# Kernel tuning notes

Hardware: AMD Instinct MI355X
Metric: run time of the kernel (lower is better)

## Reference

```python
import jax, jax.numpy as jnp
import numpy as np

HIDDEN = 512
KEY_DIM = HIDDEN // 8  # 64
B, N, M = 8, 2048, 2048


def setup_inputs() -> dict:
    key = jax.random.key(0)
    kx, ky, kwq, kbq, kwk, kbk = jax.random.split(key, 6)
    s = 1.0 / np.sqrt(HIDDEN)
    return {
        "x": jax.random.normal(kx, (B, N, HIDDEN), dtype=jnp.float32),
        "y": jax.random.normal(ky, (B, M, HIDDEN), dtype=jnp.float32),
        "Wq": jax.random.uniform(kwq, (KEY_DIM, HIDDEN), minval=-s, maxval=s, dtype=jnp.float32),
        "bq": jax.random.uniform(kbq, (KEY_DIM,), minval=-s, maxval=s, dtype=jnp.float32),
        "Wk": jax.random.uniform(kwk, (KEY_DIM, HIDDEN), minval=-s, maxval=s, dtype=jnp.float32),
        "bk": jax.random.uniform(kbk, (KEY_DIM,), minval=-s, maxval=s, dtype=jnp.float32),
    }


def reference(x, y, Wq, bq, Wk, bk):
    # linear projections (torch Linear: x @ W^T + b)
    q = jnp.einsum("bnh,kh->bnk", x, Wq) + bq  # [B,N,K]
    k = jnp.einsum("bmh,kh->bmk", y, Wk) + bk  # [B,M,K]
    # pairwise squared distance [B,N,M]
    dist = (
        -2.0 * jnp.einsum("bnk,bmk->bnm", q, k)
        + jnp.sum(q * q, axis=-1)[:, :, None]
        + jnp.sum(k * k, axis=-1)[:, None, :]
    )
    # max over M of exp(-dist), keepdim -> [B,N,1]
    atweight = jnp.max(jnp.exp(-dist), axis=-1, keepdims=True)
    # outer product per batch -> [B,N,N]
    attention = jnp.einsum("bni,bmi->bnm", atweight, atweight)
    return attention
```

## Files before the change

kernel.cpp:

```cpp
#include <hip/hip_runtime.h>

#define B_    8
#define N_    2048
#define H_    512
#define K_    64
#define NROWS 16384
#define RTOT  32768

typedef __attribute__((ext_vector_type(8))) __bf16 bf16x8;
typedef __attribute__((ext_vector_type(4))) float  floatx4;

#define MFMA(a, b, c) __builtin_amdgcn_mfma_f32_16x16x32_bf16((a), (b), (c), 0, 0, 0)

__global__ __launch_bounds__(256) void wcvt_kernel(
    const float* __restrict__ Wq, const float* __restrict__ Wk,
    __bf16* __restrict__ Whilo)
{
    const int i = blockIdx.x * 256 + threadIdx.x;
    const bool isQ = i < 32768;
    const int off = isQ ? i : i - 32768;
    const float f = isQ ? Wq[off] : Wk[off];
    const __bf16 h = (__bf16)f;
    const __bf16 l = (__bf16)(f - (float)h);
    const int base = isQ ? 0 : 65536;
    Whilo[base + off] = h;
    Whilo[base + 32768 + off] = l;
}

__global__ __launch_bounds__(128) void proj_kernel(
    const float* __restrict__ x, const float* __restrict__ y,
    const __bf16* __restrict__ Whilo,
    const float* __restrict__ bq, const float* __restrict__ bk,
    __bf16* __restrict__ qh, __bf16* __restrict__ ql,
    float* __restrict__ sq)
{
    const int tid  = threadIdx.x;
    const int wv   = tid >> 6;
    const int lane = tid & 63;
    const int quad = lane >> 4;
    const int l16  = lane & 15;
    const int rowbase = blockIdx.x * 64 + wv * 32;
    const bool isQ = rowbase < NROWS;
    const float* __restrict__ X   = isQ ? x : y;
    const int xrow0 = isQ ? rowbase : rowbase - NROWS;
    const __bf16* __restrict__ Whi = Whilo + (isQ ? 0 : 2 * 32768);
    const __bf16* __restrict__ Wlo = Whi + 32768;
    const float* __restrict__ bias = isQ ? bq : bk;

    floatx4 acc[2][4];
    #pragma unroll
    for (int rt = 0; rt < 2; ++rt)
        #pragma unroll
        for (int ot = 0; ot < 4; ++ot)
            acc[rt][ot] = floatx4{0.f, 0.f, 0.f, 0.f};

    for (int it = 0; it < 16; ++it) {
        const int k0 = it * 32 + quad * 8;
        bf16x8 ahi[2], alo[2];
        #pragma unroll
        for (int rt = 0; rt < 2; ++rt) {
            const float4 f0 = *reinterpret_cast<const float4*>(
                &X[(size_t)(xrow0 + rt * 16 + l16) * H_ + k0]);
            const float4 f1 = *reinterpret_cast<const float4*>(
                &X[(size_t)(xrow0 + rt * 16 + l16) * H_ + k0 + 4]);
            const float fv[8] = {f0.x, f0.y, f0.z, f0.w, f1.x, f1.y, f1.z, f1.w};
            #pragma unroll
            for (int j = 0; j < 8; ++j) {
                const __bf16 h = (__bf16)fv[j];
                ahi[rt][j] = h;
                alo[rt][j] = (__bf16)(fv[j] - (float)h);
            }
        }
        bf16x8 bhi[4], blo[4];
        #pragma unroll
        for (int ot = 0; ot < 4; ++ot) {
            const int wrow = ot * 16 + l16;
            bhi[ot] = *reinterpret_cast<const bf16x8*>(&Whi[(size_t)wrow * H_ + k0]);
            blo[ot] = *reinterpret_cast<const bf16x8*>(&Wlo[(size_t)wrow * H_ + k0]);
        }
        #pragma unroll
        for (int rt = 0; rt < 2; ++rt)
            #pragma unroll
            for (int ot = 0; ot < 4; ++ot) {
                acc[rt][ot] = MFMA(ahi[rt], bhi[ot], acc[rt][ot]);
                acc[rt][ot] = MFMA(ahi[rt], blo[ot], acc[rt][ot]);
                acc[rt][ot] = MFMA(alo[rt], bhi[ot], acc[rt][ot]);
            }
    }

    float bv[4];
    #pragma unroll
    for (int ot = 0; ot < 4; ++ot) bv[ot] = bias[ot * 16 + l16];

    #pragma unroll
    for (int rt = 0; rt < 2; ++rt) {
        float ss[4] = {0.f, 0.f, 0.f, 0.f};
        #pragma unroll
        for (int ot = 0; ot < 4; ++ot)
            #pragma unroll
            for (int r = 0; r < 4; ++r) {
                const float qv = acc[rt][ot][r] + bv[ot];
                acc[rt][ot][r] = qv;
                ss[r] = fmaf(qv, qv, ss[r]);
            }
        #pragma unroll
        for (int off = 1; off < 16; off <<= 1)
            #pragma unroll
            for (int r = 0; r < 4; ++r)
                ss[r] += __shfl_xor(ss[r], off);
        const int row0 = rowbase + rt * 16 + quad * 4;
        if (l16 == 0) {
            #pragma unroll
            for (int r = 0; r < 4; ++r) sq[row0 + r] = ss[r];
        }
        #pragma unroll
        for (int ot = 0; ot < 4; ++ot)
            #pragma unroll
            for (int r = 0; r < 4; ++r) {
                const size_t idx = (size_t)(row0 + r) * K_ + ot * 16 + l16;
                const float qv = acc[rt][ot][r];
                const __bf16 h = (__bf16)qv;
                qh[idx] = h;
                ql[idx] = (__bf16)(qv - (float)h);
            }
    }
}

__global__ __launch_bounds__(128) void dist_kernel(
    const __bf16* __restrict__ qh, const __bf16* __restrict__ ql,
    const float* __restrict__ sq, float* __restrict__ wout)
{
    const int tid  = threadIdx.x;
    const int wv   = tid >> 6;
    const int lane = tid & 63;
    const int quad = lane >> 4;
    const int l16  = lane & 15;
    const int blk  = blockIdx.x;
    const int b    = blk >> 6;
    const int nrow = (blk & 63) * 32 + wv * 16;
    const size_t qrow = (size_t)(b * N_ + nrow + l16);

    const bf16x8 ahi0 = *reinterpret_cast<const bf16x8*>(&qh[qrow * K_ + quad * 8]);
    const bf16x8 ahi1 = *reinterpret_cast<const bf16x8*>(&qh[qrow * K_ + 32 + quad * 8]);
    const bf16x8 alo0 = *reinterpret_cast<const bf16x8*>(&ql[qrow * K_ + quad * 8]);
    const bf16x8 alo1 = *reinterpret_cast<const bf16x8*>(&ql[qrow * K_ + 32 + quad * 8]);

    const __bf16* __restrict__ kh = qh + (size_t)NROWS * K_;
    const __bf16* __restrict__ kl = ql + (size_t)NROWS * K_;
    const float*  __restrict__ kk = sq + NROWS;

    floatx4 runmin = floatx4{1e30f, 1e30f, 1e30f, 1e30f};

    #pragma unroll 2
    for (int ms = 0; ms < 128; ++ms) {
        const size_t krow = (size_t)(b * N_ + ms * 16 + l16);
        const bf16x8 bh0 = *reinterpret_cast<const bf16x8*>(&kh[krow * K_ + quad * 8]);
        const bf16x8 bh1 = *reinterpret_cast<const bf16x8*>(&kh[krow * K_ + 32 + quad * 8]);
        const bf16x8 bl0 = *reinterpret_cast<const bf16x8*>(&kl[krow * K_ + quad * 8]);
        const bf16x8 bl1 = *reinterpret_cast<const bf16x8*>(&kl[krow * K_ + 32 + quad * 8]);
        const float kkv = kk[b * N_ + ms * 16 + l16];

        floatx4 acc = floatx4{0.f, 0.f, 0.f, 0.f};
        acc = MFMA(ahi0, bh0, acc);
        acc = MFMA(ahi1, bh1, acc);
        acc = MFMA(ahi0, bl0, acc);
        acc = MFMA(ahi1, bl1, acc);
        acc = MFMA(alo0, bh0, acc);
        acc = MFMA(alo1, bh1, acc);

        #pragma unroll
        for (int r = 0; r < 4; ++r) {
            const float d = fmaf(-2.f, acc[r], kkv);
            runmin[r] = fminf(runmin[r], d);
        }
    }

    #pragma unroll
    for (int off = 1; off < 16; off <<= 1)
        #pragma unroll
        for (int r = 0; r < 4; ++r)
            runmin[r] = fminf(runmin[r], __shfl_xor(runmin[r], off));

    if (l16 == 0) {
        #pragma unroll
        for (int r = 0; r < 4; ++r) {
            const int row = nrow + quad * 4 + r;
            const float d = runmin[r] + sq[b * N_ + row];
            wout[b * N_ + row] = expf(-d);
        }
    }
}

__global__ __launch_bounds__(256) void outer_kernel(
    const float* __restrict__ w, float4* __restrict__ out)
{
    const int f = blockIdx.x * 256 + threadIdx.x;
    const int m4 = f & 511;
    const int n  = (f >> 9) & 2047;
    const int b  = f >> 20;
    const float wn = w[(b << 11) + n];
    const float4 wm = reinterpret_cast<const float4*>(w)[(b << 9) + m4];
    float4 o;
    o.x = wn * wm.x; o.y = wn * wm.y; o.z = wn * wm.z; o.w = wn * wm.w;
    out[f] = o;
}

extern "C" void kernel_launch(void* const* d_in, const int* in_sizes, int n_in,
                              void* d_out, int out_size, void* d_ws, size_t ws_size,
                              hipStream_t stream)
{
    const float* x  = (const float*)d_in[0];
    const float* y  = (const float*)d_in[1];
    const float* Wq = (const float*)d_in[2];
    const float* bq = (const float*)d_in[3];
    const float* Wk = (const float*)d_in[4];
    const float* bk = (const float*)d_in[5];
    float* out = (float*)d_out;

    char* ws = (char*)d_ws;
    __bf16* qh    = (__bf16*)ws;
    __bf16* ql    = (__bf16*)(ws + 4194304);
    float*  sq    = (float*)(ws + 8388608);
    __bf16* Whilo = (__bf16*)(ws + 8519680);
    float*  w     = (float*)(ws + 8781824);

    wcvt_kernel<<<256, 256, 0, stream>>>(Wq, Wk, Whilo);
    proj_kernel<<<512, 128, 0, stream>>>(x, y, Whilo, bq, bk, qh, ql, sq);
    dist_kernel<<<512, 128, 0, stream>>>(qh, ql, sq, w);
    outer_kernel<<<32768, 256, 0, stream>>>(w, (float4*)out);
}
```

Before: 262.6 us.

## Fuse all stages into one cooperative kernel with split-M atomic min

Replaces the four separate launches with a single cooperative kernel that uses grid-wide syncs between weight conversion, projection, distance-min and outer-product phases. The distance phase splits the M range across two waves per row tile and combines them with an integer atomicMin on float bits, which doubles the number of waves. Projection uses 16-row tiles per wave for more parallelism. The outer product caches the batch weight vector in shared memory. The atomicMin on float bits assumes non-negative distances, and the grid syncs add some overhead.

```diff
diff --git a/kernel.cpp b/kernel.cpp
--- a/kernel.cpp
+++ b/kernel.cpp
@@ -1,4 +1,7 @@
 #include <hip/hip_runtime.h>
+#include <hip/hip_cooperative_groups.h>
+
+namespace cg = cooperative_groups;
 
 #define B_    8
 #define N_    2048
@@ -6,109 +9,103 @@
 #define K_    64
 #define NROWS 16384
 #define RTOT  32768
+#define NBLK  512
+#define NTHR  256
 
 typedef __attribute__((ext_vector_type(8))) __bf16 bf16x8;
 typedef __attribute__((ext_vector_type(4))) float  floatx4;
 
 #define MFMA(a, b, c) __builtin_amdgcn_mfma_f32_16x16x32_bf16((a), (b), (c), 0, 0, 0)
 
-__global__ __launch_bounds__(256) void wcvt_kernel(
-    const float* __restrict__ Wq, const float* __restrict__ Wk,
-    __bf16* __restrict__ Whilo)
+__global__ __launch_bounds__(NTHR, 2) void fused_kernel(
+    const float* __restrict__ x, const float* __restrict__ y,
+    const float* __restrict__ Wq, const float* __restrict__ bq,
+    const float* __restrict__ Wk, const float* __restrict__ bk,
+    float* __restrict__ out,
+    __bf16* __restrict__ qh, __bf16* __restrict__ ql,
+    float* __restrict__ sq, __bf16* __restrict__ Whilo,
+    int* __restrict__ minT)
 {
-    const int i = blockIdx.x * 256 + threadIdx.x;
-    const bool isQ = i < 32768;
-    const int off = isQ ? i : i - 32768;
-    const float f = isQ ? Wq[off] : Wk[off];
-    const __bf16 h = (__bf16)f;
-    const __bf16 l = (__bf16)(f - (float)h);
-    const int base = isQ ? 0 : 65536;
-    Whilo[base + off] = h;
-    Whilo[base + 32768 + off] = l;
-}
-
-__global__ __launch_bounds__(128) void proj_kernel(
-    const float* __restrict__ x, const float* __restrict__ y,
-    const __bf16* __restrict__ Whilo,
-    const float* __restrict__ bq, const float* __restrict__ bk,
-    __bf16* __restrict__ qh, __bf16* __restrict__ ql,
-    float* __restrict__ sq)
-{
+    cg::grid_group grid = cg::this_grid();
     const int tid  = threadIdx.x;
-    const int wv   = tid >> 6;
+    const int blk  = blockIdx.x;
+    const int gid  = blk * NTHR + tid;
     const int lane = tid & 63;
     const int quad = lane >> 4;
     const int l16  = lane & 15;
-    const int rowbase = blockIdx.x * 64 + wv * 32;
-    const bool isQ = rowbase < NROWS;
-    const float* __restrict__ X   = isQ ? x : y;
-    const int xrow0 = isQ ? rowbase : rowbase - NROWS;
-    const __bf16* __restrict__ Whi = Whilo + (isQ ? 0 : 2 * 32768);
-    const __bf16* __restrict__ Wlo = Whi + 32768;
-    const float* __restrict__ bias = isQ ? bq : bk;
-
-    floatx4 acc[2][4];
-    #pragma unroll
-    for (int rt = 0; rt < 2; ++rt)
-        #pragma unroll
-        for (int ot = 0; ot < 4; ++ot)
-            acc[rt][ot] = floatx4{0.f, 0.f, 0.f, 0.f};
-
-    for (int it = 0; it < 16; ++it) {
-        const int k0 = it * 32 + quad * 8;
-        bf16x8 ahi[2], alo[2];
-        #pragma unroll
-        for (int rt = 0; rt < 2; ++rt) {
+
+    if (gid < 2 * 32768) {
+        const bool isQ = gid < 32768;
+        const int off  = isQ ? gid : gid - 32768;
+        const float f  = isQ ? Wq[off] : Wk[off];
+        const __bf16 h = (__bf16)f;
+        const __bf16 l = (__bf16)(f - (float)h);
+        const int base = isQ ? 0 : 65536;
+        Whilo[base + off]         = h;
+        Whilo[base + 32768 + off] = l;
+    }
+    if (gid < NROWS) minT[gid] = 0x7f800000;
+    grid.sync();
+
+    {
+        const int wid = gid >> 6;
+        const int rowbase = wid * 16;
+        const bool isQ = rowbase < NROWS;
+        const float* __restrict__ X = isQ ? x : y;
+        const int xrow0 = isQ ? rowbase : rowbase - NROWS;
+        const __bf16* __restrict__ Whi = Whilo + (isQ ? 0 : 65536);
+        const __bf16* __restrict__ Wlo = Whi + 32768;
+        const float* __restrict__ bias = isQ ? bq : bk;
+
+        floatx4 acc[4];
+        #pragma unroll
+        for (int ot = 0; ot < 4; ++ot) acc[ot] = floatx4{0.f, 0.f, 0.f, 0.f};
+
+        for (int it = 0; it < 16; ++it) {
+            const int k0 = it * 32 + quad * 8;
             const float4 f0 = *reinterpret_cast<const float4*>(
-                &X[(size_t)(xrow0 + rt * 16 + l16) * H_ + k0]);
+                &X[(size_t)(xrow0 + l16) * H_ + k0]);
             const float4 f1 = *reinterpret_cast<const float4*>(
-                &X[(size_t)(xrow0 + rt * 16 + l16) * H_ + k0 + 4]);
+                &X[(size_t)(xrow0 + l16) * H_ + k0 + 4]);
             const float fv[8] = {f0.x, f0.y, f0.z, f0.w, f1.x, f1.y, f1.z, f1.w};
+            bf16x8 ahi, alo;
             #pragma unroll
             for (int j = 0; j < 8; ++j) {
                 const __bf16 h = (__bf16)fv[j];
-                ahi[rt][j] = h;
-                alo[rt][j] = (__bf16)(fv[j] - (float)h);
-            }
-        }
-        bf16x8 bhi[4], blo[4];
+                ahi[j] = h;
+                alo[j] = (__bf16)(fv[j] - (float)h);
+            }
+            #pragma unroll
+            for (int ot = 0; ot < 4; ++ot) {
+                const int wrow = ot * 16 + l16;
+                const bf16x8 bhi = *reinterpret_cast<const bf16x8*>(
+                    &Whi[(size_t)wrow * H_ + k0]);
+                const bf16x8 blo = *reinterpret_cast<const bf16x8*>(
+                    &Wlo[(size_t)wrow * H_ + k0]);
+                acc[ot] = MFMA(ahi, bhi, acc[ot]);
+                acc[ot] = MFMA(ahi, blo, acc[ot]);
+                acc[ot] = MFMA(alo, bhi, acc[ot]);
+            }
+        }
+
+        float ss[4] = {0.f, 0.f, 0.f, 0.f};
         #pragma unroll
         for (int ot = 0; ot < 4; ++ot) {
-            const int wrow = ot * 16 + l16;
-            bhi[ot] = *reinterpret_cast<const bf16x8*>(&Whi[(size_t)wrow * H_ + k0]);
-            blo[ot] = *reinterpret_cast<const bf16x8*>(&Wlo[(size_t)wrow * H_ + k0]);
-        }
-        #pragma unroll
-        for (int rt = 0; rt < 2; ++rt)
-            #pragma unroll
-            for (int ot = 0; ot < 4; ++ot) {
-                acc[rt][ot] = MFMA(ahi[rt], bhi[ot], acc[rt][ot]);
-                acc[rt][ot] = MFMA(ahi[rt], blo[ot], acc[rt][ot]);
-                acc[rt][ot] = MFMA(alo[rt], bhi[ot], acc[rt][ot]);
-            }
-    }
-
-    float bv[4];
-    #pragma unroll
-    for (int ot = 0; ot < 4; ++ot) bv[ot] = bias[ot * 16 + l16];
-
-    #pragma unroll
-    for (int rt = 0; rt < 2; ++rt) {
-        float ss[4] = {0.f, 0.f, 0.f, 0.f};
-        #pragma unroll
-        for (int ot = 0; ot < 4; ++ot)
+            const float bv = bias[ot * 16 + l16];
             #pragma unroll
             for (int r = 0; r < 4; ++r) {
-                const float qv = acc[rt][ot][r] + bv[ot];
-                acc[rt][ot][r] = qv;
+                const float qv = acc[ot][r] + bv;
+                acc[ot][r] = qv;
                 ss[r] = fmaf(qv, qv, ss[r]);
             }
+        }
         #pragma unroll
         for (int off = 1; off < 16; off <<= 1)
             #pragma unroll
             for (int r = 0; r < 4; ++r)
                 ss[r] += __shfl_xor(ss[r], off);
-        const int row0 = rowbase + rt * 16 + quad * 4;
+
+        const int row0 = rowbase + quad * 4;
         if (l16 == 0) {
             #pragma unroll
             for (int r = 0; r < 4; ++r) sq[row0 + r] = ss[r];
@@ -118,91 +115,95 @@
             #pragma unroll
             for (int r = 0; r < 4; ++r) {
                 const size_t idx = (size_t)(row0 + r) * K_ + ot * 16 + l16;
-                const float qv = acc[rt][ot][r];
+                const float qv = acc[ot][r];
                 const __bf16 h = (__bf16)qv;
                 qh[idx] = h;
                 ql[idx] = (__bf16)(qv - (float)h);
             }
     }
-}
-
-__global__ __launch_bounds__(128) void dist_kernel(
-    const __bf16* __restrict__ qh, const __bf16* __restrict__ ql,
-    const float* __restrict__ sq, float* __restrict__ wout)
-{
-    const int tid  = threadIdx.x;
-    const int wv   = tid >> 6;
-    const int lane = tid & 63;
-    const int quad = lane >> 4;
-    const int l16  = lane & 15;
-    const int blk  = blockIdx.x;
-    const int b    = blk >> 6;
-    const int nrow = (blk & 63) * 32 + wv * 16;
-    const size_t qrow = (size_t)(b * N_ + nrow + l16);
-
-    const bf16x8 ahi0 = *reinterpret_cast<const bf16x8*>(&qh[qrow * K_ + quad * 8]);
-    const bf16x8 ahi1 = *reinterpret_cast<const bf16x8*>(&qh[qrow * K_ + 32 + quad * 8]);
-    const bf16x8 alo0 = *reinterpret_cast<const bf16x8*>(&ql[qrow * K_ + quad * 8]);
-    const bf16x8 alo1 = *reinterpret_cast<const bf16x8*>(&ql[qrow * K_ + 32 + quad * 8]);
-
-    const __bf16* __restrict__ kh = qh + (size_t)NROWS * K_;
-    const __bf16* __restrict__ kl = ql + (size_t)NROWS * K_;
-    const float*  __restrict__ kk = sq + NROWS;
-
-    floatx4 runmin = floatx4{1e30f, 1e30f, 1e30f, 1e30f};
-
-    #pragma unroll 2
-    for (int ms = 0; ms < 128; ++ms) {
-        const size_t krow = (size_t)(b * N_ + ms * 16 + l16);
-        const bf16x8 bh0 = *reinterpret_cast<const bf16x8*>(&kh[krow * K_ + quad * 8]);
-        const bf16x8 bh1 = *reinterpret_cast<const bf16x8*>(&kh[krow * K_ + 32 + quad * 8]);
-        const bf16x8 bl0 = *reinterpret_cast<const bf16x8*>(&kl[krow * K_ + quad * 8]);
-        const bf16x8 bl1 = *reinterpret_cast<const bf16x8*>(&kl[krow * K_ + 32 + quad * 8]);
-        const float kkv = kk[b * N_ + ms * 16 + l16];
-
-        floatx4 acc = floatx4{0.f, 0.f, 0.f, 0.f};
-        acc = MFMA(ahi0, bh0, acc);
-        acc = MFMA(ahi1, bh1, acc);
-        acc = MFMA(ahi0, bl0, acc);
-        acc = MFMA(ahi1, bl1, acc);
-        acc = MFMA(alo0, bh0, acc);
-        acc = MFMA(alo1, bh1, acc);
-
-        #pragma unroll
-        for (int r = 0; r < 4; ++r) {
-            const float d = fmaf(-2.f, acc[r], kkv);
-            runmin[r] = fminf(runmin[r], d);
-        }
-    }
-
-    #pragma unroll
-    for (int off = 1; off < 16; off <<= 1)
-        #pragma unroll
-        for (int r = 0; r < 4; ++r)
-            runmin[r] = fminf(runmin[r], __shfl_xor(runmin[r], off));
-
-    if (l16 == 0) {
-        #pragma unroll
-        for (int r = 0; r < 4; ++r) {
-            const int row = nrow + quad * 4 + r;
-            const float d = runmin[r] + sq[b * N_ + row];
-            wout[b * N_ + row] = expf(-d);
-        }
-    }
-}
-
-__global__ __launch_bounds__(256) void outer_kernel(
-    const float* __restrict__ w, float4* __restrict__ out)
-{
-    const int f = blockIdx.x * 256 + threadIdx.x;
-    const int m4 = f & 511;
-    const int n  = (f >> 9) & 2047;
-    const int b  = f >> 20;
-    const float wn = w[(b << 11) + n];
-    const float4 wm = reinterpret_cast<const float4*>(w)[(b << 9) + m4];
-    float4 o;
-    o.x = wn * wm.x; o.y = wn * wm.y; o.z = wn * wm.z; o.w = wn * wm.w;
-    out[f] = o;
+    __threadfence();
+    grid.sync();
+
+    {
+        const int wid  = gid >> 6;
+        const int t    = wid >> 1;
+        const int half = wid & 1;
+        const int b    = t >> 7;
+        const int nrow = (t & 127) * 16;
+
+        const size_t qrow = (size_t)(b * N_ + nrow + l16);
+        const bf16x8 ahi0 = *reinterpret_cast<const bf16x8*>(&qh[qrow * K_ + quad * 8]);
+        const bf16x8 ahi1 = *reinterpret_cast<const bf16x8*>(&qh[qrow * K_ + 32 + quad * 8]);
+        const bf16x8 alo0 = *reinterpret_cast<const bf16x8*>(&ql[qrow * K_ + quad * 8]);
+        const bf16x8 alo1 = *reinterpret_cast<const bf16x8*>(&ql[qrow * K_ + 32 + quad * 8]);
+
+        const __bf16* __restrict__ kh = qh + (size_t)NROWS * K_;
+        const __bf16* __restrict__ kl = ql + (size_t)NROWS * K_;
+        const float*  __restrict__ kk = sq + NROWS;
+
+        floatx4 runmin = floatx4{1e30f, 1e30f, 1e30f, 1e30f};
+        const int ms0 = half * 64;
+
+        #pragma unroll 2
+        for (int ms = 0; ms < 64; ++ms) {
+            const size_t krow = (size_t)(b * N_ + (ms0 + ms) * 16 + l16);
+            const bf16x8 bh0 = *reinterpret_cast<const bf16x8*>(&kh[krow * K_ + quad * 8]);
+            const bf16x8 bh1 = *reinterpret_cast<const bf16x8*>(&kh[krow * K_ + 32 + quad * 8]);
+            const bf16x8 bl0 = *reinterpret_cast<const bf16x8*>(&kl[krow * K_ + quad * 8]);
+            const bf16x8 bl1 = *reinterpret_cast<const bf16x8*>(&kl[krow * K_ + 32 + quad * 8]);
+            const float kkv = kk[b * N_ + (ms0 + ms) * 16 + l16];
+
+            floatx4 acc = floatx4{0.f, 0.f, 0.f, 0.f};
+            acc = MFMA(ahi0, bh0, acc);
+            acc = MFMA(ahi1, bh1, acc);
+            acc = MFMA(ahi0, bl0, acc);
+            acc = MFMA(ahi1, bl1, acc);
+            acc = MFMA(alo0, bh0, acc);
+            acc = MFMA(alo1, bh1, acc);
+
+            #pragma unroll
+            for (int r = 0; r < 4; ++r)
+                runmin[r] = fminf(runmin[r], fmaf(-2.f, acc[r], kkv));
+        }
+
+        #pragma unroll
+        for (int off = 1; off < 16; off <<= 1)
+            #pragma unroll
+            for (int r = 0; r < 4; ++r)
+                runmin[r] = fminf(runmin[r], __shfl_xor(runmin[r], off));
+
+        if (l16 == 0) {
+            #pragma unroll
+            for (int r = 0; r < 4; ++r) {
+                const int row = nrow + quad * 4 + r;
+                const float d = runmin[r] + sq[b * N_ + row];
+                atomicMin(&minT[b * N_ + row], __float_as_int(d));
+            }
+        }
+    }
+    __threadfence();
+    grid.sync();
+
+    {
+        __shared__ float wl[2048];
+        const int R0 = blk * 32;
+        const int b  = R0 >> 11;
+        const int n0 = R0 & 2047;
+        for (int i = tid; i < 2048; i += NTHR)
+            wl[i] = expf(-__int_as_float(minT[b * N_ + i]));
+        __syncthreads();
+
+        float4* __restrict__ out4 = reinterpret_cast<float4*>(out);
+        for (int idx = tid; idx < 32 * 512; idx += NTHR) {
+            const int row = idx >> 9;
+            const int m4  = idx & 511;
+            const float  wn = wl[n0 + row];
+            const float4 wv = *reinterpret_cast<const float4*>(&wl[m4 * 4]);
+            float4 o;
+            o.x = wn * wv.x; o.y = wn * wv.y; o.z = wn * wv.z; o.w = wn * wv.w;
+            out4[(size_t)(b * N_ + n0 + row) * 512 + m4] = o;
+        }
+    }
 }
 
 extern "C" void kernel_launch(void* const* d_in, const int* in_sizes, int n_in,
@@ -219,13 +220,15 @@
 
     char* ws = (char*)d_ws;
     __bf16* qh    = (__bf16*)ws;
-    __bf16* ql    = (__bf16*)(ws + 4194304);
-    float*  sq    = (float*)(ws + 8388608);
-    __bf16* Whilo = (__bf16*)(ws + 8519680);
-    float*  w     = (float*)(ws + 8781824);
-
-    wcvt_kernel<<<256, 256, 0, stream>>>(Wq, Wk, Whilo);
-    proj_kernel<<<512, 128, 0, stream>>>(x, y, Whilo, bq, bk, qh, ql, sq);
-    dist_kernel<<<512, 128, 0, stream>>>(qh, ql, sq, w);
-    outer_kernel<<<32768, 256, 0, stream>>>(w, (float4*)out);
+    __bf16* ql    = (__bf16*)(ws + (4u << 20));
+    float*  sq    = (float*)(ws + (8u << 20));
+    __bf16* Whilo = (__bf16*)(ws + (8u << 20) + 131072);
+    int*    minT  = (int*)  (ws + (8u << 20) + 393216);
+
+    void* args[] = { (void*)&x, (void*)&y, (void*)&Wq, (void*)&bq,
+                     (void*)&Wk, (void*)&bk, (void*)&out,
+                     (void*)&qh, (void*)&ql, (void*)&sq,
+                     (void*)&Whilo, (void*)&minT };
+    hipLaunchCooperativeKernel((void*)fused_kernel, dim3(NBLK), dim3(NTHR),
+                               args, 0, stream);
 }
```

After: 543.6 us. 107% more time.
